# Kernel optimization log

Hardware: AMD Instinct MI355X
Metric: run time of the kernel (lower is better)

## Reference

```python
import jax, jax.numpy as jnp
import numpy as np

HIDDEN = 64
EXPAND = 2
INNER = HIDDEN * EXPAND
KSIZE = 4


def setup_inputs() -> dict:
    key = jax.random.key(0)
    ks = jax.random.split(key, 12)
    s = 0.02
    inp = {
        "x": jax.random.normal(ks[0], (4, 64, 1024, HIDDEN), jnp.float32),
        "w_in": jax.random.normal(ks[1], (HIDDEN, 2 * INNER), jnp.float32) * s,
        "b_in": jnp.zeros((2 * INNER,), jnp.float32),
        "w_conv": jax.random.normal(ks[2], (INNER, 1, KSIZE), jnp.float32) * s,  # depthwise: [C,1,K]
        "b_conv": jnp.zeros((INNER,), jnp.float32),
        "w_delta": jax.random.normal(ks[3], (INNER, INNER), jnp.float32) * s,
        "b_delta": jnp.zeros((INNER,), jnp.float32),
        "w_si": jax.random.normal(ks[4], (INNER, INNER), jnp.float32) * s,
        "b_si": jnp.zeros((INNER,), jnp.float32),
        "w_so": jax.random.normal(ks[5], (INNER, INNER), jnp.float32) * s,
        "b_so": jnp.zeros((INNER,), jnp.float32),
        "a_log": jnp.zeros((INNER,), jnp.float32),   # nn.Parameter(torch.zeros)
        "d_skip": jnp.ones((INNER,), jnp.float32),   # nn.Parameter(torch.ones)
        "w_out": jax.random.normal(ks[6], (INNER, HIDDEN), jnp.float32) * s,
        "b_out": jnp.zeros((HIDDEN,), jnp.float32),
    }
    return inp


def _forward(x, w_in, b_in, w_conv, b_conv, w_delta, b_delta, w_si, b_si,
             w_so, b_so, a_log, d_skip, w_out, b_out):
    B, T, N, H = x.shape
    # [B,T,N,H] -> [B*N, T, H]
    xr = jnp.transpose(x, (0, 2, 1, 3)).reshape(B * N, T, H)
    proj = xr @ w_in + b_in                      # [BN, T, 2*inner]
    signal, gate = jnp.split(proj, 2, axis=-1)
    # causal depthwise conv1d (pad left K-1, crop to T == torch pad=K-1 then [:T])
    sc = jnp.transpose(signal, (0, 2, 1))        # [BN, inner, T]
    sc = jax.lax.conv_general_dilated(
        sc, w_conv, window_strides=(1,), padding=[(KSIZE - 1, 0)],
        dimension_numbers=("NCH", "OIH", "NCH"), feature_group_count=INNER)
    sc = sc + b_conv[None, :, None]
    signal = jax.nn.silu(jnp.transpose(sc, (0, 2, 1)))  # [BN, T, inner]
    # selective scan
    delta = jax.nn.softplus(signal @ w_delta + b_delta)
    s_in = jnp.tanh(signal @ w_si + b_si)
    s_out = jnp.tanh(signal @ w_so + b_so)
    a = -jax.nn.softplus(a_log)                  # [inner]
    decay = jnp.exp(delta * a)                   # [BN, T, inner]

    def step(state, xs):
        dec_t, si_t, so_t, sg_t = xs
        state = dec_t * state + si_t * sg_t
        return state, so_t * state + d_skip * sg_t

    # time-major for scan: [T, BN, inner]
    tm = lambda t: jnp.transpose(t, (1, 0, 2))
    init = jnp.zeros((B * N, INNER), x.dtype)
    _, hidden = jax.lax.scan(step, init, (tm(decay), tm(s_in), tm(s_out), tm(signal)))
    hidden = jnp.transpose(hidden, (1, 0, 2))    # [BN, T, inner]
    hidden = hidden * jax.nn.sigmoid(gate)
    out = hidden @ w_out + b_out                 # [BN, T, H]
    return jnp.transpose(out.reshape(B, N, T, H), (0, 2, 1, 3))


def reference(x, w_in, b_in, w_conv, b_conv, w_delta, b_delta, w_si, b_si,
              w_so, b_so, a_log, d_skip, w_out, b_out):
    return _forward(x, w_in, b_in, w_conv, b_conv, w_delta, b_delta, w_si, b_si,
                    w_so, b_so, a_log, d_skip, w_out, b_out)
```

## Files before the change

kernel.cpp:

```cpp
#include <hip/hip_runtime.h>
#include <math.h>


typedef __bf16 bf16x8 __attribute__((ext_vector_type(8)));
typedef float f32x4 __attribute__((ext_vector_type(4)));

#define WIN_E 0
#define WD_E 16384
#define WSI_E 32768
#define WSO_E 49152
#define WOT_E 65536
#define WQ_END 73728
#define AS_BYTE (WQ_END * 2)

__device__ inline float sigm(float x) {
  return __builtin_amdgcn_rcpf(1.f + __expf(-x));
}
__device__ inline float tanh_c(float x) {
  return fmaf(-2.f, __builtin_amdgcn_rcpf(__expf(2.f * x) + 1.f), 1.f);
}

__device__ inline int frag_off(int col, int k, int nct) {
  int ks = k >> 5, lgk = (k >> 3) & 3, j = k & 7;
  return ((ks * nct + (col >> 4)) * 64 + ((col & 15) + (lgk << 4))) * 8 + j;
}

__global__ __launch_bounds__(256) void prep_kernel(
    const float* __restrict__ w_in, const float* __restrict__ w_delta,
    const float* __restrict__ w_si, const float* __restrict__ w_so,
    const float* __restrict__ w_out, const float* __restrict__ a_log,
    __bf16* __restrict__ wq, float* __restrict__ a_s) {
  int i = blockIdx.x * 256 + threadIdx.x;
  if (i < 16384) {
    int col = i & 255, k = i >> 8;
    wq[WIN_E + frag_off(col, k, 16)] = (__bf16)w_in[k * 256 + col];
  } else if (i < 32768) {
    int j = i - 16384, col = j & 127, k = j >> 7;
    wq[WD_E + frag_off(col, k, 8)] = (__bf16)w_delta[k * 128 + col];
  } else if (i < 49152) {
    int j = i - 32768, col = j & 127, k = j >> 7;
    wq[WSI_E + frag_off(col, k, 8)] = (__bf16)w_si[k * 128 + col];
  } else if (i < 65536) {
    int j = i - 49152, col = j & 127, k = j >> 7;
    wq[WSO_E + frag_off(col, k, 8)] = (__bf16)w_so[k * 128 + col];
  } else if (i < 73728) {
    int j = i - 65536, col = j & 63, k = j >> 6;
    wq[WOT_E + frag_off(col, k, 4)] = (__bf16)w_out[k * 64 + col];
  } else if (i < 73856) {
    int c = i - 73728;
    a_s[c] = -log1pf(__expf(a_log[c]));
  }
}

__global__ __launch_bounds__(256, 3) void mamba_main(
    const float* __restrict__ x, const float* __restrict__ b_in,
    const float* __restrict__ w_conv, const float* __restrict__ b_conv,
    const float* __restrict__ b_delta, const float* __restrict__ b_si,
    const float* __restrict__ b_so, const float* __restrict__ d_skip,
    const float* __restrict__ b_out, const __bf16* __restrict__ wqb,
    const float* __restrict__ a_s, float* __restrict__ out) {
  __shared__ __bf16 XS[32 * 72];
  __shared__ __bf16 GT[32 * 132];
  __shared__ __bf16 DH[32 * 136];
  __shared__ __bf16 HG[32 * 136];

  const int tid = threadIdx.x;
  const int lane = tid & 63;
  const int wave = tid >> 6;
  const int lr = lane & 15;
  const int lg = lane >> 4;
  const int lk = lg << 3;
  const int bb = blockIdx.x >> 10;
  const int nn = blockIdx.x & 1023;

  float bsig[2], bgat[2], bdl[2], avv[2], bsv[2], bov[2], dskv[2], cbc[2];
  float cw0[2], cw1[2], cw2[2], cw3[2];
#pragma unroll
  for (int ct = 0; ct < 2; ++ct) {
    int sc = wave * 32 + ct * 16 + lr;
    bsig[ct] = b_in[sc];
    bgat[ct] = b_in[128 + sc];
    bdl[ct] = b_delta[sc];
    avv[ct] = fminf(a_s[sc], -1e-30f);
    bsv[ct] = b_si[sc];
    bov[ct] = b_so[sc];
    dskv[ct] = d_skip[sc];
    cw0[ct] = w_conv[sc * 4 + 0];
    cw1[ct] = w_conv[sc * 4 + 1];
    cw2[ct] = w_conv[sc * 4 + 2];
    cw3[ct] = w_conv[sc * 4 + 3];
    cbc[ct] = b_conv[sc];
  }
  const float bout = b_out[wave * 16 + lr];

  float car1[2] = {0.f, 0.f}, car2[2] = {0.f, 0.f}, car3[2] = {0.f, 0.f};
  float C[2] = {0.f, 0.f};

  const int xtr = tid >> 3, xc0 = (tid & 7) * 8;
  {
    const float* xp = x + (((size_t)bb * 64 + xtr) * 1024 + nn) * 64 + xc0;
    float4 v0 = *(const float4*)xp;
    float4 v1 = *(const float4*)(xp + 4);
    bf16x8 pk;
    pk[0] = (__bf16)v0.x; pk[1] = (__bf16)v0.y; pk[2] = (__bf16)v0.z; pk[3] = (__bf16)v0.w;
    pk[4] = (__bf16)v1.x; pk[5] = (__bf16)v1.y; pk[6] = (__bf16)v1.z; pk[7] = (__bf16)v1.w;
    *(bf16x8*)(XS + xtr * 72 + xc0) = pk;
  }
  __syncthreads();

#pragma unroll
  for (int ch = 0; ch < 2; ++ch) {
    const int cbs[4] = {2 * wave, 2 * wave + 1, 8 + 2 * wave, 9 + 2 * wave};
    bf16x8 bw[4][2];
#pragma unroll
    for (int ct = 0; ct < 4; ++ct)
#pragma unroll
      for (int ks = 0; ks < 2; ++ks)
        bw[ct][ks] = *(const bf16x8*)(wqb + WIN_E + (((ks << 4) + cbs[ct]) * 64 + lane) * 8);
    float4 xv0, xv1;
    if (ch == 0) {
      const float* xp = x + (((size_t)bb * 64 + 32 + xtr) * 1024 + nn) * 64 + xc0;
      xv0 = *(const float4*)xp;
      xv1 = *(const float4*)(xp + 4);
    }
    bf16x8 ax[2][2];
#pragma unroll
    for (int mt = 0; mt < 2; ++mt)
#pragma unroll
      for (int ks = 0; ks < 2; ++ks)
        ax[mt][ks] = *(const bf16x8*)(XS + (mt * 16 + lr) * 72 + ks * 32 + lk);
    f32x4 acc[2][4];
    const f32x4 z = {0.f, 0.f, 0.f, 0.f};
#pragma unroll
    for (int mt = 0; mt < 2; ++mt)
#pragma unroll
      for (int ct = 0; ct < 4; ++ct) acc[mt][ct] = z;
#pragma unroll
    for (int ks = 0; ks < 2; ++ks)
#pragma unroll
      for (int ct = 0; ct < 4; ++ct)
#pragma unroll
        for (int mt = 0; mt < 2; ++mt)
          acc[mt][ct] = __builtin_amdgcn_mfma_f32_16x16x32_bf16(ax[mt][ks], bw[ct][ks],
                                                                acc[mt][ct], 0, 0, 0);
#pragma unroll
    for (int ct = 0; ct < 2; ++ct) {
      int gcol = wave * 32 + ct * 16 + lr;
#pragma unroll
      for (int mt = 0; mt < 2; ++mt)
#pragma unroll
        for (int r = 0; r < 4; ++r)
          GT[(mt * 16 + lg * 4 + r) * 132 + gcol] = (__bf16)sigm(acc[mt][ct + 2][r] + bgat[ct]);
    }
#pragma unroll
    for (int ct = 0; ct < 2; ++ct) {
      int col = wave * 32 + ct * 16 + lr;
      float s0 = acc[0][ct][0] + bsig[ct], s1 = acc[0][ct][1] + bsig[ct];
      float s2 = acc[0][ct][2] + bsig[ct], s3 = acc[0][ct][3] + bsig[ct];
      float t0 = acc[1][ct][0] + bsig[ct], t1 = acc[1][ct][1] + bsig[ct];
      float t2 = acc[1][ct][2] + bsig[ct], t3 = acc[1][ct][3] + bsig[ct];
      float a3 = __shfl_up(s3, 16), a2 = __shfl_up(s2, 16), a1 = __shfl_up(s1, 16);
      float p1 = lg ? a3 : car1[ct];
      float p2 = lg ? a2 : car2[ct];
      float p3 = lg ? a1 : car3[ct];
      float b3 = __shfl_up(t3, 16), b2 = __shfl_up(t2, 16), b1 = __shfl_up(t1, 16);
      float q15 = __shfl(s3, lr + 48), q14 = __shfl(s2, lr + 48), q13 = __shfl(s1, lr + 48);
      float e1 = lg ? b3 : q15;
      float e2 = lg ? b2 : q14;
      float e3 = lg ? b1 : q13;
      car1[ct] = __shfl(t3, lr + 48);
      car2[ct] = __shfl(t2, lr + 48);
      car3[ct] = __shfl(t1, lr + 48);
      float c0 = fmaf(cw0[ct], p3, fmaf(cw1[ct], p2, fmaf(cw2[ct], p1, fmaf(cw3[ct], s0, cbc[ct]))));
      float c1 = fmaf(cw0[ct], p2, fmaf(cw1[ct], p1, fmaf(cw2[ct], s0, fmaf(cw3[ct], s1, cbc[ct]))));
      float c2 = fmaf(cw0[ct], p1, fmaf(cw1[ct], s0, fmaf(cw2[ct], s1, fmaf(cw3[ct], s2, cbc[ct]))));
      float c3 = fmaf(cw0[ct], s0, fmaf(cw1[ct], s1, fmaf(cw2[ct], s2, fmaf(cw3[ct], s3, cbc[ct]))));
      float d0 = fmaf(cw0[ct], e3, fmaf(cw1[ct], e2, fmaf(cw2[ct], e1, fmaf(cw3[ct], t0, cbc[ct]))));
      float d1 = fmaf(cw0[ct], e2, fmaf(cw1[ct], e1, fmaf(cw2[ct], t0, fmaf(cw3[ct], t1, cbc[ct]))));
      float d2 = fmaf(cw0[ct], e1, fmaf(cw1[ct], t0, fmaf(cw2[ct], t1, fmaf(cw3[ct], t2, cbc[ct]))));
      float d3 = fmaf(cw0[ct], t0, fmaf(cw1[ct], t1, fmaf(cw2[ct], t2, fmaf(cw3[ct], t3, cbc[ct]))));
      DH[(lg * 4 + 0) * 136 + col] = (__bf16)(c0 * sigm(c0));
      DH[(lg * 4 + 1) * 136 + col] = (__bf16)(c1 * sigm(c1));
      DH[(lg * 4 + 2) * 136 + col] = (__bf16)(c2 * sigm(c2));
      DH[(lg * 4 + 3) * 136 + col] = (__bf16)(c3 * sigm(c3));
      DH[(16 + lg * 4 + 0) * 136 + col] = (__bf16)(d0 * sigm(d0));
      DH[(16 + lg * 4 + 1) * 136 + col] = (__bf16)(d1 * sigm(d1));
      DH[(16 + lg * 4 + 2) * 136 + col] = (__bf16)(d2 * sigm(d2));
      DH[(16 + lg * 4 + 3) * 136 + col] = (__bf16)(d3 * sigm(d3));
    }
    __syncthreads();

    bf16x8 af[2][4];
#pragma unroll
    for (int mt = 0; mt < 2; ++mt)
#pragma unroll
      for (int ks = 0; ks < 4; ++ks)
        af[mt][ks] = *(const bf16x8*)(DH + (mt * 16 + lr) * 136 + ks * 32 + lk);
    if (ch == 0) {
      bf16x8 pk;
      pk[0] = (__bf16)xv0.x; pk[1] = (__bf16)xv0.y; pk[2] = (__bf16)xv0.z; pk[3] = (__bf16)xv0.w;
      pk[4] = (__bf16)xv1.x; pk[5] = (__bf16)xv1.y; pk[6] = (__bf16)xv1.z; pk[7] = (__bf16)xv1.w;
      *(bf16x8*)(XS + xtr * 72 + xc0) = pk;
    }
#pragma unroll
    for (int ct = 0; ct < 2; ++ct) {
      const int col = wave * 32 + ct * 16 + lr;
      const int cb = 2 * wave + ct;
      const f32x4 zz = {0.f, 0.f, 0.f, 0.f};
      bf16x8 bfr[4];
#pragma unroll
      for (int ks = 0; ks < 4; ++ks)
        bfr[ks] = *(const bf16x8*)(wqb + WD_E + (((ks << 3) + cb) * 64 + lane) * 8);
      f32x4 ad[2] = {zz, zz};
#pragma unroll
      for (int ks = 0; ks < 4; ++ks)
#pragma unroll
        for (int mt = 0; mt < 2; ++mt)
          ad[mt] = __builtin_amdgcn_mfma_f32_16x16x32_bf16(af[mt][ks], bfr[ks], ad[mt], 0, 0, 0);
      float dec[2][4];
#pragma unroll
      for (int mt = 0; mt < 2; ++mt)
#pragma unroll
        for (int r = 0; r < 4; ++r) {
          float xd = ad[mt][r] + bdl[ct];
          dec[mt][r] = __expf(avv[ct] * __logf(1.f + __expf(xd)));
        }
#pragma unroll
      for (int ks = 0; ks < 4; ++ks)
        bfr[ks] = *(const bf16x8*)(wqb + WSI_E + (((ks << 3) + cb) * 64 + lane) * 8);
      f32x4 as_[2] = {zz, zz};
#pragma unroll
      for (int ks = 0; ks < 4; ++ks)
#pragma unroll
        for (int mt = 0; mt < 2; ++mt)
          as_[mt] = __builtin_amdgcn_mfma_f32_16x16x32_bf16(af[mt][ks], bfr[ks], as_[mt], 0, 0, 0);
      float sg[2][4], u[2][4];
#pragma unroll
      for (int mt = 0; mt < 2; ++mt)
#pragma unroll
        for (int r = 0; r < 4; ++r) {
          sg[mt][r] = (float)DH[(mt * 16 + lg * 4 + r) * 136 + col];
          u[mt][r] = tanh_c(as_[mt][r] + bsv[ct]) * sg[mt][r];
        }
      float p0 = u[0][0];
      float p1s = fmaf(dec[0][1], p0, u[0][1]);
      float p2s = fmaf(dec[0][2], p1s, u[0][2]);
      float p3s = fmaf(dec[0][3], p2s, u[0][3]);
      float Q0 = dec[0][0], Q1 = Q0 * dec[0][1], Q2 = Q1 * dec[0][2], Q3 = Q2 * dec[0][3];
      float r0 = u[1][0];
      float r1s = fmaf(dec[1][1], r0, u[1][1]);
      float r2s = fmaf(dec[1][2], r1s, u[1][2]);
      float r3s = fmaf(dec[1][3], r2s, u[1][3]);
      float S0 = dec[1][0], S1 = S0 * dec[1][1], S2 = S1 * dec[1][2], S3 = S2 * dec[1][3];
#pragma unroll
      for (int ks = 0; ks < 4; ++ks)
        bfr[ks] = *(const bf16x8*)(wqb + WSO_E + (((ks << 3) + cb) * 64 + lane) * 8);
      f32x4 ao[2] = {zz, zz};
#pragma unroll
      for (int ks = 0; ks < 4; ++ks)
#pragma unroll
        for (int mt = 0; mt < 2; ++mt)
          ao[mt] = __builtin_amdgcn_mfma_f32_16x16x32_bf16(af[mt][ks], bfr[ks], ao[mt], 0, 0, 0);
      float tao[2][4];
#pragma unroll
      for (int mt = 0; mt < 2; ++mt)
#pragma unroll
        for (int r = 0; r < 4; ++r) tao[mt][r] = tanh_c(ao[mt][r] + bov[ct]);
      float Pa = Q3, La = p3s;
      float shp = __shfl_up(Pa, 16), shl = __shfl_up(La, 16);
      float Pa1 = (lg >= 1) ? Pa * shp : Pa;
      float La1 = (lg >= 1) ? fmaf(Pa, shl, La) : La;
      shp = __shfl_up(Pa1, 32); shl = __shfl_up(La1, 32);
      float Pa2 = (lg >= 2) ? Pa1 * shp : Pa1;
      float La2 = (lg >= 2) ? fmaf(Pa1, shl, La1) : La1;
      shp = __shfl_up(Pa2, 16); shl = __shfl_up(La2, 16);
      float Sin0 = lg ? fmaf(shp, C[ct], shl) : C[ct];
      float Pb = __shfl(Pa2, lr + 48), Lb = __shfl(La2, lr + 48);
      float T0 = fmaf(Pb, C[ct], Lb);
      float Pc = S3, Lc = r3s;
      shp = __shfl_up(Pc, 16); shl = __shfl_up(Lc, 16);
      float Pc1 = (lg >= 1) ? Pc * shp : Pc;
      float Lc1 = (lg >= 1) ? fmaf(Pc, shl, Lc) : Lc;
      shp = __shfl_up(Pc1, 32); shl = __shfl_up(Lc1, 32);
      float Pc2 = (lg >= 2) ? Pc1 * shp : Pc1;
      float Lc2 = (lg >= 2) ? fmaf(Pc1, shl, Lc1) : Lc1;
      shp = __shfl_up(Pc2, 16); shl = __shfl_up(Lc2, 16);
      float Sin1 = lg ? fmaf(shp, T0, shl) : T0;
      float Pd = __shfl(Pc2, lr + 48), Ld = __shfl(Lc2, lr + 48);
      C[ct] = fmaf(Pd, T0, Ld);
      float st00 = fmaf(Q0, Sin0, p0);
      float st01 = fmaf(Q1, Sin0, p1s);
      float st02 = fmaf(Q2, Sin0, p2s);
      float st03 = fmaf(Q3, Sin0, p3s);
      float st10 = fmaf(S0, Sin1, r0);
      float st11 = fmaf(S1, Sin1, r1s);
      float st12 = fmaf(S2, Sin1, r2s);
      float st13 = fmaf(S3, Sin1, r3s);
      float stv[2][4] = {{st00, st01, st02, st03}, {st10, st11, st12, st13}};
#pragma unroll
      for (int mt = 0; mt < 2; ++mt)
#pragma unroll
        for (int r = 0; r < 4; ++r) {
          int row = mt * 16 + lg * 4 + r;
          float sigv = (float)GT[row * 132 + col];
          float h = sigv * fmaf(tao[mt][r], stv[mt][r], dskv[ct] * sg[mt][r]);
          HG[row * 136 + col] = (__bf16)h;
        }
    }
    bf16x8 bw5[4];
#pragma unroll
    for (int ks = 0; ks < 4; ++ks)
      bw5[ks] = *(const bf16x8*)(wqb + WOT_E + (((ks << 2) + wave) * 64 + lane) * 8);
    __syncthreads();

    {
      bf16x8 ah[2][4];
#pragma unroll
      for (int mt = 0; mt < 2; ++mt)
#pragma unroll
        for (int ks = 0; ks < 4; ++ks)
          ah[mt][ks] = *(const bf16x8*)(HG + (mt * 16 + lr) * 136 + ks * 32 + lk);
      const f32x4 zz = {0.f, 0.f, 0.f, 0.f};
      f32x4 a5[2] = {zz, zz};
#pragma unroll
      for (int ks = 0; ks < 4; ++ks)
#pragma unroll
        for (int mt = 0; mt < 2; ++mt)
          a5[mt] = __builtin_amdgcn_mfma_f32_16x16x32_bf16(ah[mt][ks], bw5[ks], a5[mt], 0, 0, 0);
      size_t ob = (((size_t)bb * 64 + ch * 32) * 1024 + nn) * 64 + wave * 16 + lr;
#pragma unroll
      for (int mt = 0; mt < 2; ++mt)
#pragma unroll
        for (int r = 0; r < 4; ++r)
          out[ob + (size_t)(mt * 16 + lg * 4 + r) * 65536] = a5[mt][r] + bout;
    }
  }
}

extern "C" void kernel_launch(void* const* d_in, const int* in_sizes, int n_in,
                              void* d_out, int out_size, void* d_ws, size_t ws_size,
                              hipStream_t stream) {
  const float* x = (const float*)d_in[0];
  const float* w_in = (const float*)d_in[1];
  const float* b_in = (const float*)d_in[2];
  const float* w_conv = (const float*)d_in[3];
  const float* b_conv = (const float*)d_in[4];
  const float* w_delta = (const float*)d_in[5];
  const float* b_delta = (const float*)d_in[6];
  const float* w_si = (const float*)d_in[7];
  const float* b_si = (const float*)d_in[8];
  const float* w_so = (const float*)d_in[9];
  const float* b_so = (const float*)d_in[10];
  const float* a_log = (const float*)d_in[11];
  const float* d_skip = (const float*)d_in[12];
  const float* w_out = (const float*)d_in[13];
  const float* b_out = (const float*)d_in[14];

  __bf16* wq = (__bf16*)d_ws;
  float* a_s = (float*)((char*)d_ws + AS_BYTE);

  hipLaunchKernelGGL(prep_kernel, dim3(289), dim3(256), 0, stream,
                     w_in, w_delta, w_si, w_so, w_out, a_log, wq, a_s);
  hipLaunchKernelGGL(mamba_main, dim3(4096), dim3(256), 0, stream,
                     x, b_in, w_conv, b_conv, b_delta, b_si, b_so, d_skip, b_out,
                     wq, a_s, (float*)d_out);
}
```

Baseline: 121.9 us.

## Keep gate and signal in registers, use exp2 transcendentals, raise occupancy

Drops the GT shared-memory buffer and keeps sigmoid(gate) and the silu'd signal values in registers. This removes the LDS write/read round trip for the gate and the bf16 reload of the signal. Sigmoid, tanh, softplus and exp are rewritten around native exp2/log2 intrinsics, with the LOG2E scaling folded into the biases. The launch bound goes from 3 to 4 blocks per SM, which together with the smaller LDS footprint aims at more waves in flight. The cost is more live registers under a tighter register cap, which may cause spills.

```diff
diff --git a/kernel.cpp b/kernel.cpp
--- a/kernel.cpp
+++ b/kernel.cpp
@@ -4,6 +4,8 @@
 
 typedef __bf16 bf16x8 __attribute__((ext_vector_type(8)));
 typedef float f32x4 __attribute__((ext_vector_type(4)));
+
+#define LOG2E 1.44269504088896f
 
 #define WIN_E 0
 #define WD_E 16384
@@ -13,13 +15,9 @@
 #define WQ_END 73728
 #define AS_BYTE (WQ_END * 2)
 
-__device__ inline float sigm(float x) {
-  return __builtin_amdgcn_rcpf(1.f + __expf(-x));
-}
-__device__ inline float tanh_c(float x) {
-  return fmaf(-2.f, __builtin_amdgcn_rcpf(__expf(2.f * x) + 1.f), 1.f);
-}
-
+__device__ inline float sigm2(float xnL) {
+  return __builtin_amdgcn_rcpf(1.f + __builtin_amdgcn_exp2f(xnL));
+}
 __device__ inline int frag_off(int col, int k, int nct) {
   int ks = k >> 5, lgk = (k >> 3) & 3, j = k & 7;
   return ((ks * nct + (col >> 4)) * 64 + ((col & 15) + (lgk << 4))) * 8 + j;
@@ -52,7 +50,7 @@
   }
 }
 
-__global__ __launch_bounds__(256, 3) void mamba_main(
+__global__ __launch_bounds__(256, 4) void mamba_main(
     const float* __restrict__ x, const float* __restrict__ b_in,
     const float* __restrict__ w_conv, const float* __restrict__ b_conv,
     const float* __restrict__ b_delta, const float* __restrict__ b_si,
@@ -60,7 +58,6 @@
     const float* __restrict__ b_out, const __bf16* __restrict__ wqb,
     const float* __restrict__ a_s, float* __restrict__ out) {
   __shared__ __bf16 XS[32 * 72];
-  __shared__ __bf16 GT[32 * 132];
   __shared__ __bf16 DH[32 * 136];
   __shared__ __bf16 HG[32 * 136];
 
@@ -73,17 +70,17 @@
   const int bb = blockIdx.x >> 10;
   const int nn = blockIdx.x & 1023;
 
-  float bsig[2], bgat[2], bdl[2], avv[2], bsv[2], bov[2], dskv[2], cbc[2];
+  float bsig[2], bgatnL[2], bdlL[2], avv[2], bsv2L[2], bov2L[2], dskv[2], cbc[2];
   float cw0[2], cw1[2], cw2[2], cw3[2];
 #pragma unroll
   for (int ct = 0; ct < 2; ++ct) {
     int sc = wave * 32 + ct * 16 + lr;
     bsig[ct] = b_in[sc];
-    bgat[ct] = b_in[128 + sc];
-    bdl[ct] = b_delta[sc];
+    bgatnL[ct] = -LOG2E * b_in[128 + sc];
+    bdlL[ct] = LOG2E * b_delta[sc];
     avv[ct] = fminf(a_s[sc], -1e-30f);
-    bsv[ct] = b_si[sc];
-    bov[ct] = b_so[sc];
+    bsv2L[ct] = 2.f * LOG2E * b_si[sc];
+    bov2L[ct] = 2.f * LOG2E * b_so[sc];
     dskv[ct] = d_skip[sc];
     cw0[ct] = w_conv[sc * 4 + 0];
     cw1[ct] = w_conv[sc * 4 + 1];
@@ -95,6 +92,8 @@
 
   float car1[2] = {0.f, 0.f}, car2[2] = {0.f, 0.f}, car3[2] = {0.f, 0.f};
   float C[2] = {0.f, 0.f};
+  float sgv[2][2][4];
+  float sigg[2][2][4];
 
   const int xtr = tid >> 3, xc0 = (tid & 7) * 8;
   {
@@ -144,14 +143,12 @@
           acc[mt][ct] = __builtin_amdgcn_mfma_f32_16x16x32_bf16(ax[mt][ks], bw[ct][ks],
                                                                 acc[mt][ct], 0, 0, 0);
 #pragma unroll
-    for (int ct = 0; ct < 2; ++ct) {
-      int gcol = wave * 32 + ct * 16 + lr;
+    for (int ct = 0; ct < 2; ++ct)
 #pragma unroll
       for (int mt = 0; mt < 2; ++mt)
 #pragma unroll
         for (int r = 0; r < 4; ++r)
-          GT[(mt * 16 + lg * 4 + r) * 132 + gcol] = (__bf16)sigm(acc[mt][ct + 2][r] + bgat[ct]);
-    }
+          sigg[ct][mt][r] = sigm2(fmaf(acc[mt][ct + 2][r], -LOG2E, bgatnL[ct]));
 #pragma unroll
     for (int ct = 0; ct < 2; ++ct) {
       int col = wave * 32 + ct * 16 + lr;
@@ -171,22 +168,25 @@
       car1[ct] = __shfl(t3, lr + 48);
       car2[ct] = __shfl(t2, lr + 48);
       car3[ct] = __shfl(t1, lr + 48);
-      float c0 = fmaf(cw0[ct], p3, fmaf(cw1[ct], p2, fmaf(cw2[ct], p1, fmaf(cw3[ct], s0, cbc[ct]))));
-      float c1 = fmaf(cw0[ct], p2, fmaf(cw1[ct], p1, fmaf(cw2[ct], s0, fmaf(cw3[ct], s1, cbc[ct]))));
-      float c2 = fmaf(cw0[ct], p1, fmaf(cw1[ct], s0, fmaf(cw2[ct], s1, fmaf(cw3[ct], s2, cbc[ct]))));
-      float c3 = fmaf(cw0[ct], s0, fmaf(cw1[ct], s1, fmaf(cw2[ct], s2, fmaf(cw3[ct], s3, cbc[ct]))));
-      float d0 = fmaf(cw0[ct], e3, fmaf(cw1[ct], e2, fmaf(cw2[ct], e1, fmaf(cw3[ct], t0, cbc[ct]))));
-      float d1 = fmaf(cw0[ct], e2, fmaf(cw1[ct], e1, fmaf(cw2[ct], t0, fmaf(cw3[ct], t1, cbc[ct]))));
-      float d2 = fmaf(cw0[ct], e1, fmaf(cw1[ct], t0, fmaf(cw2[ct], t1, fmaf(cw3[ct], t2, cbc[ct]))));
-      float d3 = fmaf(cw0[ct], t0, fmaf(cw1[ct], t1, fmaf(cw2[ct], t2, fmaf(cw3[ct], t3, cbc[ct]))));
-      DH[(lg * 4 + 0) * 136 + col] = (__bf16)(c0 * sigm(c0));
-      DH[(lg * 4 + 1) * 136 + col] = (__bf16)(c1 * sigm(c1));
-      DH[(lg * 4 + 2) * 136 + col] = (__bf16)(c2 * sigm(c2));
-      DH[(lg * 4 + 3) * 136 + col] = (__bf16)(c3 * sigm(c3));
-      DH[(16 + lg * 4 + 0) * 136 + col] = (__bf16)(d0 * sigm(d0));
-      DH[(16 + lg * 4 + 1) * 136 + col] = (__bf16)(d1 * sigm(d1));
-      DH[(16 + lg * 4 + 2) * 136 + col] = (__bf16)(d2 * sigm(d2));
-      DH[(16 + lg * 4 + 3) * 136 + col] = (__bf16)(d3 * sigm(d3));
+      float cv[4], dv[4];
+      cv[0] = fmaf(cw0[ct], p3, fmaf(cw1[ct], p2, fmaf(cw2[ct], p1, fmaf(cw3[ct], s0, cbc[ct]))));
+      cv[1] = fmaf(cw0[ct], p2, fmaf(cw1[ct], p1, fmaf(cw2[ct], s0, fmaf(cw3[ct], s1, cbc[ct]))));
+      cv[2] = fmaf(cw0[ct], p1, fmaf(cw1[ct], s0, fmaf(cw2[ct], s1, fmaf(cw3[ct], s2, cbc[ct]))));
+      cv[3] = fmaf(cw0[ct], s0, fmaf(cw1[ct], s1, fmaf(cw2[ct], s2, fmaf(cw3[ct], s3, cbc[ct]))));
+      dv[0] = fmaf(cw0[ct], e3, fmaf(cw1[ct], e2, fmaf(cw2[ct], e1, fmaf(cw3[ct], t0, cbc[ct]))));
+      dv[1] = fmaf(cw0[ct], e2, fmaf(cw1[ct], e1, fmaf(cw2[ct], t0, fmaf(cw3[ct], t1, cbc[ct]))));
+      dv[2] = fmaf(cw0[ct], e1, fmaf(cw1[ct], t0, fmaf(cw2[ct], t1, fmaf(cw3[ct], t2, cbc[ct]))));
+      dv[3] = fmaf(cw0[ct], t0, fmaf(cw1[ct], t1, fmaf(cw2[ct], t2, fmaf(cw3[ct], t3, cbc[ct]))));
+#pragma unroll
+      for (int r = 0; r < 4; ++r) {
+        float c = cv[r], d = dv[r];
+        float vc = c * sigm2(c * -LOG2E);
+        float vd = d * sigm2(d * -LOG2E);
+        sgv[ct][0][r] = vc;
+        sgv[ct][1][r] = vd;
+        DH[(lg * 4 + r) * 136 + col] = (__bf16)vc;
+        DH[(16 + lg * 4 + r) * 136 + col] = (__bf16)vd;
+      }
     }
     __syncthreads();
 
@@ -222,8 +222,8 @@
       for (int mt = 0; mt < 2; ++mt)
 #pragma unroll
         for (int r = 0; r < 4; ++r) {
-          float xd = ad[mt][r] + bdl[ct];
-          dec[mt][r] = __expf(avv[ct] * __logf(1.f + __expf(xd)));
+          float t = __builtin_amdgcn_exp2f(fmaf(ad[mt][r], LOG2E, bdlL[ct]));
+          dec[mt][r] = __builtin_amdgcn_exp2f(avv[ct] * __builtin_amdgcn_logf(1.f + t));
         }
 #pragma unroll
       for (int ks = 0; ks < 4; ++ks)
@@ -234,13 +234,14 @@
 #pragma unroll
         for (int mt = 0; mt < 2; ++mt)
           as_[mt] = __builtin_amdgcn_mfma_f32_16x16x32_bf16(af[mt][ks], bfr[ks], as_[mt], 0, 0, 0);
-      float sg[2][4], u[2][4];
+      float u[2][4];
 #pragma unroll
       for (int mt = 0; mt < 2; ++mt)
 #pragma unroll
         for (int r = 0; r < 4; ++r) {
-          sg[mt][r] = (float)DH[(mt * 16 + lg * 4 + r) * 136 + col];
-          u[mt][r] = tanh_c(as_[mt][r] + bsv[ct]) * sg[mt][r];
+          float e = __builtin_amdgcn_exp2f(fmaf(as_[mt][r], 2.f * LOG2E, bsv2L[ct]));
+          float th = fmaf(-2.f, __builtin_amdgcn_rcpf(1.f + e), 1.f);
+          u[mt][r] = th * sgv[ct][mt][r];
         }
       float p0 = u[0][0];
       float p1s = fmaf(dec[0][1], p0, u[0][1]);
@@ -265,7 +266,10 @@
 #pragma unroll
       for (int mt = 0; mt < 2; ++mt)
 #pragma unroll
-        for (int r = 0; r < 4; ++r) tao[mt][r] = tanh_c(ao[mt][r] + bov[ct]);
+        for (int r = 0; r < 4; ++r) {
+          float e = __builtin_amdgcn_exp2f(fmaf(ao[mt][r], 2.f * LOG2E, bov2L[ct]));
+          tao[mt][r] = fmaf(-2.f, __builtin_amdgcn_rcpf(1.f + e), 1.f);
+        }
       float Pa = Q3, La = p3s;
       float shp = __shfl_up(Pa, 16), shl = __shfl_up(La, 16);
       float Pa1 = (lg >= 1) ? Pa * shp : Pa;
@@ -288,22 +292,22 @@
       float Sin1 = lg ? fmaf(shp, T0, shl) : T0;
       float Pd = __shfl(Pc2, lr + 48), Ld = __shfl(Lc2, lr + 48);
       C[ct] = fmaf(Pd, T0, Ld);
-      float st00 = fmaf(Q0, Sin0, p0);
-      float st01 = fmaf(Q1, Sin0, p1s);
-      float st02 = fmaf(Q2, Sin0, p2s);
-      float st03 = fmaf(Q3, Sin0, p3s);
-      float st10 = fmaf(S0, Sin1, r0);
-      float st11 = fmaf(S1, Sin1, r1s);
-      float st12 = fmaf(S2, Sin1, r2s);
-      float st13 = fmaf(S3, Sin1, r3s);
-      float stv[2][4] = {{st00, st01, st02, st03}, {st10, st11, st12, st13}};
+      float stv[2][4];
+      stv[0][0] = fmaf(Q0, Sin0, p0);
+      stv[0][1] = fmaf(Q1, Sin0, p1s);
+      stv[0][2] = fmaf(Q2, Sin0, p2s);
+      stv[0][3] = fmaf(Q3, Sin0, p3s);
+      stv[1][0] = fmaf(S0, Sin1, r0);
+      stv[1][1] = fmaf(S1, Sin1, r1s);
+      stv[1][2] = fmaf(S2, Sin1, r2s);
+      stv[1][3] = fmaf(S3, Sin1, r3s);
 #pragma unroll
       for (int mt = 0; mt < 2; ++mt)
 #pragma unroll
         for (int r = 0; r < 4; ++r) {
           int row = mt * 16 + lg * 4 + r;
-          float sigv = (float)GT[row * 132 + col];
-          float h = sigv * fmaf(tao[mt][r], stv[mt][r], dskv[ct] * sg[mt][r]);
+          float h = sigg[ct][mt][r] *
+                    fmaf(tao[mt][r], stv[mt][r], dskv[ct] * sgv[ct][mt][r]);
           HG[row * 136 + col] = (__bf16)h;
         }
     }
```

New measurement: 197.5 us. +62.0%, slower.
